# Optimization experiments

Hardware: AMD Instinct MI355X
Metric: run time of the kernel (lower is better)

## Reference

```python
import jax, jax.numpy as jnp
import numpy as np

N, C, W = 16, 512, 4096          # batch lines, channels, max width (frames)
FINAL_DIM = 512
MASK_WIDTH = 4
NUM_NEGATIVES = 10
NUM_MASKS = 256                  # ~ mask_prob * T_total / mask_width


def _build_static():
    # Deterministic ragged lengths, already descending (pack_padded_sequence order).
    seq_len = (W - 128 * np.arange(N)).astype(np.int64)       # [4096, 3968, ..., 2176]
    t = np.arange(W)[:, None]                                  # time-major outer axis
    b = np.arange(N)[None, :]
    valid = seq_len[None, :] > t                               # [W, N]
    # pack_padded_sequence layout: for each t, all batches with len>t (desc length order)
    pack_idx = ((b * W + t)[valid]).astype(np.int64)           # [T_total] indices into flat (N*W)
    T = pack_idx.shape[0]                                      # 50176
    n_blocks = T // MASK_WIDTH
    rng = np.random.default_rng(0)
    perm = rng.permutation(n_blocks)
    sel1 = np.sort(perm[:NUM_MASKS])
    sel2 = np.sort(perm[NUM_MASKS:NUM_MASKS + NUM_NEGATIVES * NUM_MASKS])
    off = np.arange(MASK_WIDTH)
    # non-overlapping contiguous mask_width blocks, ascending (boolean-mask gather order)
    masked_idx = (sel1[:, None] * MASK_WIDTH + off).ravel().astype(np.int64)   # mask == 1
    neg_idx = (sel2[:, None] * MASK_WIDTH + off).ravel().astype(np.int64)      # mask == 2
    return seq_len, pack_idx, masked_idx, neg_idx


def setup_inputs() -> dict:
    key = jax.random.key(0)
    k1, k2, k3 = jax.random.split(key, 3)
    seq_len, pack_idx, masked_idx, neg_idx = _build_static()
    inputs = jax.random.normal(k1, (N, C, 1, W), dtype=jnp.float32)
    mask_emb = jax.random.normal(k2, (MASK_WIDTH, C), dtype=jnp.float32) * 0.02
    Wq = jax.random.normal(k3, (FINAL_DIM, C), dtype=jnp.float32) * (1.0 / np.sqrt(C))
    bq = jnp.zeros((FINAL_DIM,), dtype=jnp.float32)
    return {
        'inputs': inputs,
        'seq_len': jnp.asarray(seq_len, jnp.int32),
        'pack_idx': jnp.asarray(pack_idx, jnp.int32),
        'masked_idx': jnp.asarray(masked_idx, jnp.int32),
        'neg_idx': jnp.asarray(neg_idx, jnp.int32),
        'mask_emb': mask_emb,
        'Wq': Wq,
        'bq': bq,
    }


def reference(inputs, seq_len, pack_idx, masked_idx, neg_idx, mask_emb, Wq, bq):
    Nn, Cc, H, Ww = inputs.shape                              # H == 1
    # (N, C, 1, W) -> (N, W, 1, C) -> flat (N*W, C)
    x = jnp.transpose(inputs, (0, 3, 2, 1)).reshape(Nn * Ww, Cc)
    packed = x[pack_idx]                                      # [T_total, C] packed (time-major)
    # project_q on masked (mask==1) and negative (mask==2) token groups
    unmasked = (packed[masked_idx] @ Wq.T + bq).reshape(1, NUM_MASKS, MASK_WIDTH, FINAL_DIM)
    negatives = (packed[neg_idx] @ Wq.T + bq).reshape(NUM_NEGATIVES, NUM_MASKS, MASK_WIDTH, FINAL_DIM)
    # overwrite masked positions with the repeated mask embedding table
    packed = packed.at[masked_idx].set(jnp.tile(mask_emb, (NUM_MASKS, 1)))
    # pad_packed_sequence: scatter back to padded (N, W, C), zeros elsewhere
    out = jnp.zeros((Nn * Ww, Cc), dtype=inputs.dtype).at[pack_idx].set(packed)
    out = out.reshape(Nn, Ww, Cc).transpose(0, 2, 1)[:, :, None, :]   # (N, C, 1, W)
    return out, unmasked, negatives
```

## Files before the change

kernel.cpp:

```cpp
#include <hip/hip_runtime.h>

#define NB 16
#define CC 512
#define WW 4096
#define FD 512
#define NMASK 1024
#define T_COMB 11264
#define OUT0_ELEMS (NB*CC*WW)

#define WS_LOOKUP_OFF 0
#define WS_WQ_OFF     262144
#define WS_A_OFF      786432

#define S_LDS 36

typedef __attribute__((ext_vector_type(8))) short short8;
typedef __attribute__((ext_vector_type(4))) float f32x4;
typedef __attribute__((ext_vector_type(4))) unsigned short u16x4;

__device__ __forceinline__ unsigned short f2bf(float x) {
  unsigned int u = __builtin_bit_cast(unsigned int, x);
  u += 0x7fffu + ((u >> 16) & 1u);
  return (unsigned short)(u >> 16);
}

__device__ __forceinline__ void gload_lds16(const void* gp, void* lp) {
  __builtin_amdgcn_global_load_lds(
      (__attribute__((address_space(1))) void*)(gp),
      (__attribute__((address_space(3))) void*)(lp),
      16, 0, 0);
}

__global__ __launch_bounds__(256) void scatter_lookup_k(
    const int* __restrict__ pack_idx, const int* __restrict__ masked_idx,
    const int* __restrict__ neg_idx, int* __restrict__ lookup) {
  int g = blockIdx.x * 256 + threadIdx.x;
  int pidx = (g < NMASK) ? masked_idx[g] : neg_idx[g - NMASK];
  lookup[pack_idx[pidx]] = g;
}

__global__ __launch_bounds__(256) void fused_copy_k(
    const float* __restrict__ in, const int* __restrict__ seq_len,
    const int* __restrict__ lookup, const float* __restrict__ mask_emb,
    const float* __restrict__ Wq, float* __restrict__ out0,
    unsigned short* __restrict__ A_ws, unsigned short* __restrict__ Wq_ws) {
  if (blockIdx.x >= 2048) {
    int b2 = blockIdx.x - 2048;
    const f32x4* wq4 = (const f32x4*)Wq;
#pragma unroll
    for (int it = 0; it < 4; ++it) {
      int i4 = it * 16384 + b2 * 256 + (int)threadIdx.x;
      f32x4 v = wq4[i4];
      u16x4 o;
      o[0] = f2bf(v[0]); o[1] = f2bf(v[1]); o[2] = f2bf(v[2]); o[3] = f2bf(v[3]);
      ((u16x4*)Wq_ws)[i4] = o;
    }
    return;
  }
  const int tid = threadIdx.x;
  const int bx = blockIdx.x;
  const int n = bx >> 7;
  const int w0 = (bx & 127) * 32;
  const int wl4 = (tid & 7) * 4;
  const int w = w0 + wl4;
  const int c0 = tid >> 3;
  const size_t rowbase = ((size_t)n << 21) + (size_t)w;
  f32x4* out4 = (f32x4*)out0;
  const int L = seq_len[n];

  if (w0 + 32 > L) {
    f32x4 z = {0.f, 0.f, 0.f, 0.f};
#pragma unroll
    for (int it = 0; it < 16; ++it) {
      int c = it * 32 + c0;
      __builtin_nontemporal_store(z, &out4[(rowbase + ((size_t)c << 12)) >> 2]);
    }
    return;
  }

  __shared__ unsigned short tile[CC * S_LDS];
  __shared__ int g_s[32];
  if (tid < 32) g_s[tid] = lookup[n * WW + w0 + tid];

  const int4 g4 = *(const int4*)&lookup[n * WW + w];
  const int gg[4] = {g4.x, g4.y, g4.z, g4.w};
  bool lane_has_mask = ((unsigned)gg[0] < (unsigned)NMASK) |
                       ((unsigned)gg[1] < (unsigned)NMASK) |
                       ((unsigned)gg[2] < (unsigned)NMASK) |
                       ((unsigned)gg[3] < (unsigned)NMASK);
  bool lane_has_sel = (gg[0] >= 0) | (gg[1] >= 0) | (gg[2] >= 0) | (gg[3] >= 0);
  bool has_mask = __ballot(lane_has_mask) != 0ull;
  bool has_sel = __ballot(lane_has_sel) != 0ull;

  const f32x4* in4 = (const f32x4*)in;
#pragma unroll
  for (int it = 0; it < 16; ++it) {
    int c = it * 32 + c0;
    size_t i4 = (rowbase + ((size_t)c << 12)) >> 2;
    f32x4 v = __builtin_nontemporal_load(&in4[i4]);
    if (has_sel) {
      u16x4 bf;
      bf[0] = f2bf(v[0]); bf[1] = f2bf(v[1]);
      bf[2] = f2bf(v[2]); bf[3] = f2bf(v[3]);
      *(u16x4*)&tile[c * S_LDS + wl4] = bf;
    }
    if (has_mask) {
      float o[4] = {v[0], v[1], v[2], v[3]};
#pragma unroll
      for (int k = 0; k < 4; ++k)
        if ((unsigned)gg[k] < (unsigned)NMASK)
          o[k] = mask_emb[(gg[k] & 3) * CC + c];
      v[0] = o[0]; v[1] = o[1]; v[2] = o[2]; v[3] = o[3];
    }
    __builtin_nontemporal_store(v, &out4[i4]);
  }
  if (!has_sel) return;
  __syncthreads();

  const int lane = tid & 63;
  bool sel = (lane < 32) && (g_s[lane & 31] >= 0);
  unsigned smask = (unsigned)__ballot(sel);
  const int c2 = tid * 2;
  while (smask) {
    int wl = __builtin_ctz(smask);
    smask &= smask - 1;
    int g = g_s[wl];
    ushort2 val;
    val.x = tile[c2 * S_LDS + wl];
    val.y = tile[(c2 + 1) * S_LDS + wl];
    *(ushort2*)&A_ws[(size_t)g * CC + c2] = val;
  }
}

__global__ __launch_bounds__(256) void gemm_k(
    const unsigned short* __restrict__ A, const unsigned short* __restrict__ B,
    const float* __restrict__ bq, float* __restrict__ out) {
  __shared__ unsigned short As[2][64 * 64];
  __shared__ unsigned short Bs[2][128 * 64];
  const int tid = threadIdx.x;
  const int lane = tid & 63;
  const int quad = lane >> 4;
  const int r16 = lane & 15;
  const int wv = tid >> 6;
  const int bm = blockIdx.x * 64;
  const int bf = blockIdx.y * 128;
  const int wm = (wv & 1) * 32;
  const int wf = (wv >> 1) * 64;
  const int wbase = tid & ~63;

  f32x4 acc[2][4];
#pragma unroll
  for (int mi = 0; mi < 2; ++mi)
#pragma unroll
    for (int fi = 0; fi < 4; ++fi)
      acc[mi][fi] = (f32x4){0.f, 0.f, 0.f, 0.f};

#define STAGE_TILES(buf, k0)                                                  \
  do {                                                                        \
    _Pragma("unroll")                                                         \
    for (int it = 0; it < 2; ++it) {                                          \
      int ch = it * 256 + tid;                                                \
      int row = ch >> 3;                                                      \
      int l = (ch & 7) ^ (row & 7);                                           \
      gload_lds16(A + (size_t)(bm + row) * 512 + (k0) + l * 8,                \
                  &As[buf][(it * 256 + wbase) * 8]);                          \
    }                                                                         \
    _Pragma("unroll")                                                         \
    for (int it = 0; it < 4; ++it) {                                          \
      int ch = it * 256 + tid;                                                \
      int row = ch >> 3;                                                      \
      int l = (ch & 7) ^ (row & 7);                                           \
      gload_lds16(B + (size_t)(bf + row) * 512 + (k0) + l * 8,                \
                  &Bs[buf][(it * 256 + wbase) * 8]);                          \
    }                                                                         \
  } while (0)

  STAGE_TILES(0, 0);
  __syncthreads();

#pragma unroll
  for (int t = 0; t < 8; ++t) {
    const int cur = t & 1;
    if (t < 7) STAGE_TILES(cur ^ 1, (t + 1) * 64);

    short8 a[2][2], b[4][2];
#pragma unroll
    for (int mi = 0; mi < 2; ++mi) {
      int row = wm + mi * 16 + r16;
      int base = row * 64;
      int rx = (row & 7) << 3;
#pragma unroll
      for (int ks = 0; ks < 2; ++ks)
        a[mi][ks] = *(const short8*)&As[cur][base + ((((ks * 4 + quad) << 3)) ^ rx)];
    }
#pragma unroll
    for (int fi = 0; fi < 4; ++fi) {
      int row = wf + fi * 16 + r16;
      int base = row * 64;
      int rx = (row & 7) << 3;
#pragma unroll
      for (int ks = 0; ks < 2; ++ks)
        b[fi][ks] = *(const short8*)&Bs[cur][base + ((((ks * 4 + quad) << 3)) ^ rx)];
    }
#pragma unroll
    for (int ks = 0; ks < 2; ++ks)
#pragma unroll
      for (int mi = 0; mi < 2; ++mi)
#pragma unroll
        for (int fi = 0; fi < 4; ++fi)
          acc[mi][fi] = __builtin_amdgcn_mfma_f32_16x16x32_bf16(
              a[mi][ks], b[fi][ks], acc[mi][fi], 0, 0, 0);
    __syncthreads();
  }
#undef STAGE_TILES

#pragma unroll
  for (int fi = 0; fi < 4; ++fi) {
    int f = bf + wf + fi * 16 + r16;
    float bqv = bq[f];
#pragma unroll
    for (int mi = 0; mi < 2; ++mi) {
      int m0 = bm + wm + mi * 16 + quad * 4;
#pragma unroll
      for (int r = 0; r < 4; ++r)
        __builtin_nontemporal_store(acc[mi][fi][r] + bqv,
                                    &out[(size_t)(m0 + r) * 512 + f]);
    }
  }
}

extern "C" void kernel_launch(void* const* d_in, const int* in_sizes, int n_in,
                              void* d_out, int out_size, void* d_ws, size_t ws_size,
                              hipStream_t stream) {
  const float* inputs    = (const float*)d_in[0];
  const int*   seq_len   = (const int*)d_in[1];
  const int*   pack_idx  = (const int*)d_in[2];
  const int*   masked_idx= (const int*)d_in[3];
  const int*   neg_idx   = (const int*)d_in[4];
  const float* mask_emb  = (const float*)d_in[5];
  const float* Wq        = (const float*)d_in[6];
  const float* bq        = (const float*)d_in[7];
  float* out = (float*)d_out;
  char* ws = (char*)d_ws;
  int* lookup = (int*)(ws + WS_LOOKUP_OFF);
  unsigned short* wqb = (unsigned short*)(ws + WS_WQ_OFF);
  unsigned short* aws = (unsigned short*)(ws + WS_A_OFF);

  (void)hipMemsetAsync(lookup, 0xFF, NB * WW * sizeof(int), stream);
  scatter_lookup_k<<<44, 256, 0, stream>>>(pack_idx, masked_idx, neg_idx, lookup);
  fused_copy_k<<<2112, 256, 0, stream>>>(inputs, seq_len, lookup, mask_emb, Wq,
                                         out, aws, wqb);
  gemm_k<<<dim3(176, 4), 256, 0, stream>>>(aws, wqb, bq, out + OUT0_ELEMS);
}
```

Baseline: 285.1 us.

## Load GEMM MFMA fragments directly from global into registers, dropping LDS staging

The GEMM kernel no longer stages A and B tiles through shared memory with global_load_lds and barriers. Each wave now loads its own MFMA fragments straight from global memory into double-buffered registers, prefetching the next k-step. This removes the LDS round trip and the __syncthreads per k-step, but waves no longer share loaded data, so redundant global and L2 traffic rises and register pressure grows.

```diff
diff --git a/kernel.cpp b/kernel.cpp
--- a/kernel.cpp
+++ b/kernel.cpp
@@ -22,13 +22,6 @@
   unsigned int u = __builtin_bit_cast(unsigned int, x);
   u += 0x7fffu + ((u >> 16) & 1u);
   return (unsigned short)(u >> 16);
-}
-
-__device__ __forceinline__ void gload_lds16(const void* gp, void* lp) {
-  __builtin_amdgcn_global_load_lds(
-      (__attribute__((address_space(1))) void*)(gp),
-      (__attribute__((address_space(3))) void*)(lp),
-      16, 0, 0);
 }
 
 __global__ __launch_bounds__(256) void scatter_lookup_k(
@@ -135,8 +128,6 @@
 __global__ __launch_bounds__(256) void gemm_k(
     const unsigned short* __restrict__ A, const unsigned short* __restrict__ B,
     const float* __restrict__ bq, float* __restrict__ out) {
-  __shared__ unsigned short As[2][64 * 64];
-  __shared__ unsigned short Bs[2][128 * 64];
   const int tid = threadIdx.x;
   const int lane = tid & 63;
   const int quad = lane >> 4;
@@ -146,7 +137,9 @@
   const int bf = blockIdx.y * 128;
   const int wm = (wv & 1) * 32;
   const int wf = (wv >> 1) * 64;
-  const int wbase = tid & ~63;
+
+  const unsigned short* ap = A + (size_t)(bm + wm + r16) * 512 + quad * 8;
+  const unsigned short* bp = B + (size_t)(bf + wf + r16) * 512 + quad * 8;
 
   f32x4 acc[2][4];
 #pragma unroll
@@ -155,53 +148,29 @@
     for (int fi = 0; fi < 4; ++fi)
       acc[mi][fi] = (f32x4){0.f, 0.f, 0.f, 0.f};
 
-#define STAGE_TILES(buf, k0)                                                  \
+  short8 a[2][2][2], b[2][4][2];
+
+#define LOAD_FRAGS(buf, k0)                                                   \
   do {                                                                        \
     _Pragma("unroll")                                                         \
-    for (int it = 0; it < 2; ++it) {                                          \
-      int ch = it * 256 + tid;                                                \
-      int row = ch >> 3;                                                      \
-      int l = (ch & 7) ^ (row & 7);                                           \
-      gload_lds16(A + (size_t)(bm + row) * 512 + (k0) + l * 8,                \
-                  &As[buf][(it * 256 + wbase) * 8]);                          \
-    }                                                                         \
+    for (int mi = 0; mi < 2; ++mi)                                            \
+      _Pragma("unroll")                                                       \
+      for (int ks = 0; ks < 2; ++ks)                                          \
+        a[buf][mi][ks] =                                                      \
+            *(const short8*)(ap + (size_t)mi * (16 * 512) + (k0) + ks * 32);  \
     _Pragma("unroll")                                                         \
-    for (int it = 0; it < 4; ++it) {                                          \
-      int ch = it * 256 + tid;                                                \
-      int row = ch >> 3;                                                      \
-      int l = (ch & 7) ^ (row & 7);                                           \
-      gload_lds16(B + (size_t)(bf + row) * 512 + (k0) + l * 8,                \
-                  &Bs[buf][(it * 256 + wbase) * 8]);                          \
-    }                                                                         \
+    for (int fi = 0; fi < 4; ++fi)                                            \
+      _Pragma("unroll")                                                       \
+      for (int ks = 0; ks < 2; ++ks)                                          \
+        b[buf][fi][ks] =                                                      \
+            *(const short8*)(bp + (size_t)fi * (16 * 512) + (k0) + ks * 32);  \
   } while (0)
 
-  STAGE_TILES(0, 0);
-  __syncthreads();
-
+  LOAD_FRAGS(0, 0);
 #pragma unroll
   for (int t = 0; t < 8; ++t) {
     const int cur = t & 1;
-    if (t < 7) STAGE_TILES(cur ^ 1, (t + 1) * 64);
-
-    short8 a[2][2], b[4][2];
-#pragma unroll
-    for (int mi = 0; mi < 2; ++mi) {
-      int row = wm + mi * 16 + r16;
-      int base = row * 64;
-      int rx = (row & 7) << 3;
-#pragma unroll
-      for (int ks = 0; ks < 2; ++ks)
-        a[mi][ks] = *(const short8*)&As[cur][base + ((((ks * 4 + quad) << 3)) ^ rx)];
-    }
-#pragma unroll
-    for (int fi = 0; fi < 4; ++fi) {
-      int row = wf + fi * 16 + r16;
-      int base = row * 64;
-      int rx = (row & 7) << 3;
-#pragma unroll
-      for (int ks = 0; ks < 2; ++ks)
-        b[fi][ks] = *(const short8*)&Bs[cur][base + ((((ks * 4 + quad) << 3)) ^ rx)];
-    }
+    if (t < 7) LOAD_FRAGS(cur ^ 1, (t + 1) * 64);
 #pragma unroll
     for (int ks = 0; ks < 2; ++ks)
 #pragma unroll
@@ -209,10 +178,9 @@
 #pragma unroll
         for (int fi = 0; fi < 4; ++fi)
           acc[mi][fi] = __builtin_amdgcn_mfma_f32_16x16x32_bf16(
-              a[mi][ks], b[fi][ks], acc[mi][fi], 0, 0, 0);
-    __syncthreads();
-  }
-#undef STAGE_TILES
+              a[cur][mi][ks], b[cur][fi][ks], acc[mi][fi], 0, 0, 0);
+  }
+#undef LOAD_FRAGS
 
 #pragma unroll
   for (int fi = 0; fi < 4; ++fi) {
```

Measured after the change: 306.2 us. 1.07x slower.
